# Kernel tuning notes

Measured on AMD Instinct MI355X. Metric: run time of the kernel, lower is better.

Reference implementation:

```python
import jax, jax.numpy as jnp
import numpy as np

B, S, D, H = 2, 2048, 1024, 16
DK = D // H

def setup_inputs() -> dict:
    key = jax.random.key(0)
    ks = jax.random.split(key, 12)
    scale = 1.0 / np.sqrt(D)
    inp = {
        'q': jax.random.normal(ks[0], (B, S, D), jnp.float32),
        'k': jax.random.normal(ks[1], (B, S, D), jnp.float32),
        'v': jax.random.normal(ks[2], (B, S, D), jnp.float32),
        # causal mask: 1 where attending is allowed (j <= i), 0 for future tokens
        'mask': jnp.tril(jnp.ones((S, S), jnp.int32))[None, None, :, :],
        'wq': jax.random.normal(ks[3], (D, D), jnp.float32) * scale,
        'bq': jnp.zeros((D,), jnp.float32),
        'wk': jax.random.normal(ks[4], (D, D), jnp.float32) * scale,
        'bk': jnp.zeros((D,), jnp.float32),
        'wv': jax.random.normal(ks[5], (D, D), jnp.float32) * scale,
        'bv': jnp.zeros((D,), jnp.float32),
        'wo': jax.random.normal(ks[6], (D, D), jnp.float32) * scale,
        'bo': jnp.zeros((D,), jnp.float32),
    }
    return inp


def reference(q, k, v, mask, wq, bq, wk, bk, wv, bv, wo, bo):
    def split_heads(x):
        # [B,S,D] -> [B,H,S,DK]
        return x.reshape(B, S, H, DK).transpose(0, 2, 1, 3)

    query = split_heads(q @ wq + bq)
    key_ = split_heads(k @ wk + bk)
    value = split_heads(v @ wv + bv)

    # [B,H,S,S] attention scores
    scores = jnp.einsum('bhqd,bhkd->bhqk', query, key_) / jnp.sqrt(
        jnp.asarray(DK, jnp.float32))
    scores = jnp.where(mask == 0, jnp.asarray(-1e9, scores.dtype), scores)
    attn = jax.nn.softmax(scores, axis=-1)  # dropout p=0.0 (eval mode)

    x = jnp.einsum('bhqk,bhkd->bhqd', attn, value)  # [B,H,S,DK]
    x = x.transpose(0, 2, 1, 3).reshape(B, S, D)
    return x @ wo + bo
```

## Files before the change

kernel.cpp:

```cpp
#include <hip/hip_runtime.h>
#include <hip/hip_bf16.h>

#define BATCH 2
#define SEQ   2048
#define DMODEL 1024
#define NHEAD 16
#define DK    64
#define MTOK  (BATCH * SEQ)

typedef __attribute__((ext_vector_type(8))) short bf16x8;
typedef __attribute__((ext_vector_type(4))) float f32x4;

__device__ __forceinline__ unsigned short f2bf(float x) {
    unsigned u = __float_as_uint(x);
    u = (u + 0x7FFFu + ((u >> 16) & 1u)) >> 16;
    return (unsigned short)u;
}

__device__ __forceinline__ void store_out(float* p, float v)          { *p = v; }
__device__ __forceinline__ void store_out(unsigned short* p, float v) { *p = f2bf(v); }

__device__ __forceinline__ void g2lds16(const void* g, void* l) {
    __builtin_amdgcn_global_load_lds(
        (const __attribute__((address_space(1))) void*)g,
        (__attribute__((address_space(3))) void*)l, 16, 0, 0);
}

__global__ __launch_bounds__(256) void cvt3_bf16_kernel(
    const float* __restrict__ s0, const float* __restrict__ s1,
    const float* __restrict__ s2,
    unsigned short* __restrict__ d0, unsigned short* __restrict__ d1,
    unsigned short* __restrict__ d2, int n)
{
    const float* src; unsigned short* dst;
    switch (blockIdx.z) {
        case 0:  src = s0; dst = d0; break;
        case 1:  src = s1; dst = d1; break;
        default: src = s2; dst = d2; break;
    }
    int i = (blockIdx.x * 256 + threadIdx.x) * 8;
    if (i >= n) return;
    float4 a = *(const float4*)(src + i);
    float4 b = *(const float4*)(src + i + 4);
    union { unsigned short s[8]; uint4 u; } o;
    o.s[0] = f2bf(a.x); o.s[1] = f2bf(a.y); o.s[2] = f2bf(a.z); o.s[3] = f2bf(a.w);
    o.s[4] = f2bf(b.x); o.s[5] = f2bf(b.y); o.s[6] = f2bf(b.z); o.s[7] = f2bf(b.w);
    *(uint4*)(dst + i) = o.u;
}

__global__ __launch_bounds__(256) void wtrans_kernel(
    const float* __restrict__ w0, const float* __restrict__ w1,
    const float* __restrict__ w2, const float* __restrict__ w3,
    unsigned short* __restrict__ t0, unsigned short* __restrict__ t1,
    unsigned short* __restrict__ t2, unsigned short* __restrict__ t3)
{
    __shared__ float tile[32][33];
    const float* W; unsigned short* T;
    switch (blockIdx.z) {
        case 0:  W = w0; T = t0; break;
        case 1:  W = w1; T = t1; break;
        case 2:  W = w2; T = t2; break;
        default: W = w3; T = t3; break;
    }
    const int n0 = blockIdx.x * 32, k0 = blockIdx.y * 32;
    const int t  = threadIdx.x;
    const int r  = t >> 3;
    const int c4 = (t & 7) * 4;

    float4 v = *(const float4*)&W[(size_t)(k0 + r) * DMODEL + n0 + c4];
    tile[r][c4 + 0] = v.x; tile[r][c4 + 1] = v.y;
    tile[r][c4 + 2] = v.z; tile[r][c4 + 3] = v.w;
    __syncthreads();

    union { unsigned short s[4]; uint2 u; } o;
#pragma unroll
    for (int u = 0; u < 4; ++u) o.s[u] = f2bf(tile[c4 + u][r]);
    *(uint2*)&T[(size_t)(n0 + r) * DMODEL + k0 + c4] = o.u;
}

struct Gemm3 {
    const unsigned short* A[3];
    const unsigned short* Bt[3];
    const float* bias[3];
    void* C[3];
};

template <typename OutT>
__global__ __launch_bounds__(256) void gemm_lds_kernel(Gemm3 g, int M, int N, int K)
{
    __shared__ unsigned short sA[16 * 512];
    __shared__ unsigned short sB[16 * 512];

    const int z = blockIdx.z;
    const unsigned short* __restrict__ A  = g.A[z];
    const unsigned short* __restrict__ Bt = g.Bt[z];
    const float* __restrict__ bias = g.bias[z];
    OutT* __restrict__ C = (OutT*)g.C[z];

    const int t    = threadIdx.x;
    const int w    = t >> 6;
    const int lane = t & 63;
    const int ln   = lane & 15;
    const int qg   = lane >> 4;
    const int wm   = w >> 1;
    const int wn   = w & 1;
    const int row0 = blockIdx.y * 128;
    const int col0 = blockIdx.x * 128;

    const unsigned short* sp[8];
    unsigned short* lp[8];
#pragma unroll
    for (int i = 0; i < 8; ++i) {
        const int s = w * 8 + i;
        if (s < 16) {
            const int mtg = s >> 1, kc = s & 1;
            sp[i] = A + (size_t)(row0 + mtg * 16 + ln) * K + kc * 32 + qg * 8;
            lp[i] = &sA[s * 512];
        } else {
            const int bi = s - 16;
            const int ntg = bi >> 1, kc = bi & 1;
            sp[i] = Bt + (size_t)(col0 + ntg * 16 + ln) * K + kc * 32 + qg * 8;
            lp[i] = &sB[bi * 512];
        }
    }

    f32x4 acc[4][4];
#pragma unroll
    for (int mt = 0; mt < 4; ++mt)
#pragma unroll
        for (int nt = 0; nt < 4; ++nt) acc[mt][nt] = (f32x4){0.f, 0.f, 0.f, 0.f};

    for (int kt = 0; kt < K / 64; ++kt) {
        __syncthreads();
        const int koff = kt * 64;
#pragma unroll
        for (int i = 0; i < 8; ++i)
            g2lds16(sp[i] + koff, lp[i]);
        __syncthreads();

#pragma unroll
        for (int kc = 0; kc < 2; ++kc) {
            bf16x8 aF[4], bF[4];
#pragma unroll
            for (int mt = 0; mt < 4; ++mt)
                aF[mt] = *(const bf16x8*)&sA[(((wm * 4 + mt) * 2) + kc) * 512 + lane * 8];
#pragma unroll
            for (int nt = 0; nt < 4; ++nt)
                bF[nt] = *(const bf16x8*)&sB[(((wn * 4 + nt) * 2) + kc) * 512 + lane * 8];
#pragma unroll
            for (int mt = 0; mt < 4; ++mt)
#pragma unroll
                for (int nt = 0; nt < 4; ++nt)
                    acc[mt][nt] = __builtin_amdgcn_mfma_f32_16x16x32_bf16(
                        aF[mt], bF[nt], acc[mt][nt], 0, 0, 0);
        }
    }

    float bfv[4];
#pragma unroll
    for (int nt = 0; nt < 4; ++nt)
        bfv[nt] = bias[col0 + wn * 64 + nt * 16 + ln];

#pragma unroll
    for (int mt = 0; mt < 4; ++mt)
#pragma unroll
        for (int nt = 0; nt < 4; ++nt)
#pragma unroll
            for (int r = 0; r < 4; ++r) {
                int row = row0 + wm * 64 + mt * 16 + qg * 4 + r;
                int col = col0 + wn * 64 + nt * 16 + ln;
                store_out(&C[(size_t)row * N + col], acc[mt][nt][r] + bfv[nt]);
            }
}

#define BR 64
#define BC 64
#define PSTR 72

__global__ __launch_bounds__(256, 4) void attn_mfma_kernel(
    const unsigned short* __restrict__ Qg, const unsigned short* __restrict__ Kg,
    const unsigned short* __restrict__ Vg, unsigned short* __restrict__ O)
{
    __shared__ unsigned short sQ[8 * 512];
    __shared__ unsigned short sK[8 * 512];
    __shared__ unsigned short sVt[DK * 64];
    __shared__ unsigned short sP[BR * PSTR];

    const int t    = threadIdx.x;
    const int w    = t >> 6;
    const int lane = t & 63;
    const int ln   = lane & 15;
    const int qg   = lane >> 4;

    const int id  = blockIdx.x;
    const int bh  = id & 31;
    const int qt  = (SEQ / BR - 1) - (id >> 5);
    const int b   = bh >> 4;
    const int h   = bh & 15;
    const int qi0 = qt * BR;

    const size_t rowbase = (size_t)b * SEQ;
    const size_t colbase = (size_t)h * DK;

#pragma unroll
    for (int i = 0; i < 2; ++i) {
        const int s = w * 2 + i;
        const unsigned short* gp =
            Qg + (rowbase + qi0 + w * 16 + ln) * DMODEL + colbase + i * 32 + qg * 8;
        g2lds16(gp, &sQ[s * 512]);
    }
    __syncthreads();

    bf16x8 aq[2];
#pragma unroll
    for (int kc = 0; kc < 2; ++kc)
        aq[kc] = *(const bf16x8*)&sQ[(w * 2 + kc) * 512 + lane * 8];

    f32x4 ofrag[4];
#pragma unroll
    for (int nt = 0; nt < 4; ++nt) ofrag[nt] = (f32x4){0.f, 0.f, 0.f, 0.f};
    float m_r[4], l_r[4];
#pragma unroll
    for (int r = 0; r < 4; ++r) { m_r[r] = -3.0e38f; l_r[r] = 0.f; }

    for (int j0 = 0; j0 <= qi0; j0 += BC) {
        __syncthreads();

#pragma unroll
        for (int i = 0; i < 2; ++i) {
            const int s  = w * 2 + i;
            const int nt = s >> 1, kc = s & 1;
            const unsigned short* gp =
                Kg + (rowbase + j0 + nt * 16 + ln) * DMODEL + colbase + kc * 32 + qg * 8;
            g2lds16(gp, &sK[s * 512]);
        }
#pragma unroll
        for (int it = 0; it < 2; ++it) {
            int chunk = t + 256 * it;
            int r  = chunk >> 3;
            int c  = (chunk & 7) * 8;
            int ci = chunk & 7;
            union { uint4 u; unsigned short s[8]; } d;
            d.u = *(const uint4*)&Vg[(rowbase + j0 + r) * DMODEL + colbase + c];
#pragma unroll
            for (int u = 0; u < 8; ++u)
                sVt[(c + u) * 64 + (r ^ (ci * 8))] = d.s[u];
        }
        __syncthreads();

        f32x4 sf[4];
#pragma unroll
        for (int nt = 0; nt < 4; ++nt) {
            f32x4 a2 = (f32x4){0.f, 0.f, 0.f, 0.f};
#pragma unroll
            for (int kc = 0; kc < 2; ++kc) {
                bf16x8 bk = *(const bf16x8*)&sK[(nt * 2 + kc) * 512 + lane * 8];
                a2 = __builtin_amdgcn_mfma_f32_16x16x32_bf16(aq[kc], bk, a2, 0, 0, 0);
            }
            sf[nt] = a2;
        }

        const bool diag = (j0 == qi0);
#pragma unroll
        for (int nt = 0; nt < 4; ++nt)
#pragma unroll
            for (int r = 0; r < 4; ++r) {
                float x = sf[nt][r] * 0.125f;
                if (diag) {
                    int qrow = w * 16 + qg * 4 + r;
                    int col  = nt * 16 + ln;
                    if (col > qrow) x = -3.0e38f;
                }
                sf[nt][r] = x;
            }

        float rmax[4];
#pragma unroll
        for (int r = 0; r < 4; ++r)
            rmax[r] = fmaxf(fmaxf(sf[0][r], sf[1][r]), fmaxf(sf[2][r], sf[3][r]));
#pragma unroll
        for (int off = 8; off >= 1; off >>= 1)
#pragma unroll
            for (int r = 0; r < 4; ++r)
                rmax[r] = fmaxf(rmax[r], __shfl_xor(rmax[r], off));

        float alpha[4];
#pragma unroll
        for (int r = 0; r < 4; ++r) {
            float mn = fmaxf(m_r[r], rmax[r]);
            alpha[r] = __expf(m_r[r] - mn);
            m_r[r] = mn;
        }

        float pf[4][4];
        float rsum[4] = {0.f, 0.f, 0.f, 0.f};
#pragma unroll
        for (int nt = 0; nt < 4; ++nt)
#pragma unroll
            for (int r = 0; r < 4; ++r) {
                float p = __expf(sf[nt][r] - m_r[r]);
                pf[nt][r] = p;
                rsum[r] += p;
            }
#pragma unroll
        for (int off = 8; off >= 1; off >>= 1)
#pragma unroll
            for (int r = 0; r < 4; ++r)
                rsum[r] += __shfl_xor(rsum[r], off);
#pragma unroll
        for (int r = 0; r < 4; ++r) l_r[r] = l_r[r] * alpha[r] + rsum[r];
#pragma unroll
        for (int nt = 0; nt < 4; ++nt)
#pragma unroll
            for (int r = 0; r < 4; ++r) ofrag[nt][r] *= alpha[r];

#pragma unroll
        for (int nt = 0; nt < 4; ++nt)
#pragma unroll
            for (int r = 0; r < 4; ++r) {
                int row = w * 16 + qg * 4 + r;
                int col = (nt * 16 + ln) ^ (((w * 4 + qg) & 7) * 8);
                sP[row * PSTR + col] = f2bf(pf[nt][r]);
            }

        bf16x8 apf[2];
#pragma unroll
        for (int kc = 0; kc < 2; ++kc) {
            int row = w * 16 + ln;
            int col = (kc * 32 + qg * 8) ^ ((((row >> 2) & 7)) * 8);
            apf[kc] = *(const bf16x8*)&sP[row * PSTR + col];
        }

#pragma unroll
        for (int nt = 0; nt < 4; ++nt) {
#pragma unroll
            for (int kc = 0; kc < 2; ++kc) {
                int dk = nt * 16 + ln;
                int ci = (dk >> 3) & 7;
                bf16x8 bv = *(const bf16x8*)&sVt[dk * 64 + ((kc * 32 + qg * 8) ^ (ci * 8))];
                ofrag[nt] = __builtin_amdgcn_mfma_f32_16x16x32_bf16(apf[kc], bv, ofrag[nt], 0, 0, 0);
            }
        }
    }

#pragma unroll
    for (int nt = 0; nt < 4; ++nt)
#pragma unroll
        for (int r = 0; r < 4; ++r) {
            int gq = qi0 + w * 16 + qg * 4 + r;
            O[(rowbase + gq) * DMODEL + colbase + nt * 16 + ln] =
                f2bf(ofrag[nt][r] / l_r[r]);
        }
}

extern "C" void kernel_launch(void* const* d_in, const int* in_sizes, int n_in,
                              void* d_out, int out_size, void* d_ws, size_t ws_size,
                              hipStream_t stream)
{
    const float* q  = (const float*)d_in[0];
    const float* k  = (const float*)d_in[1];
    const float* v  = (const float*)d_in[2];
    const float* wq = (const float*)d_in[4];
    const float* bq = (const float*)d_in[5];
    const float* wk = (const float*)d_in[6];
    const float* bk = (const float*)d_in[7];
    const float* wv = (const float*)d_in[8];
    const float* bv = (const float*)d_in[9];
    const float* wo = (const float*)d_in[10];
    const float* bo = (const float*)d_in[11];
    float* out = (float*)d_out;

    const size_t mat  = (size_t)MTOK * DMODEL;
    const size_t wmat = (size_t)DMODEL * DMODEL;
    unsigned short* Abq = (unsigned short*)d_ws;
    unsigned short* Abk = Abq + mat;
    unsigned short* Abv = Abk + mat;
    unsigned short* WtQ = Abv + mat;
    unsigned short* WtK = WtQ + wmat;
    unsigned short* WtV = WtK + wmat;
    unsigned short* WtO = WtV + wmat;
    unsigned short* Qb  = WtO + wmat;
    unsigned short* Kb  = Qb + mat;
    unsigned short* Vb  = Kb + mat;
    unsigned short* CTX = Vb + mat;

    cvt3_bf16_kernel<<<dim3((unsigned)(mat / 2048), 1, 3), 256, 0, stream>>>(
        q, k, v, Abq, Abk, Abv, (int)mat);
    wtrans_kernel<<<dim3(32, 32, 4), 256, 0, stream>>>(wq, wk, wv, wo, WtQ, WtK, WtV, WtO);

    Gemm3 gqkv;
    gqkv.A[0] = Abq; gqkv.A[1] = Abk; gqkv.A[2] = Abv;
    gqkv.Bt[0] = WtQ; gqkv.Bt[1] = WtK; gqkv.Bt[2] = WtV;
    gqkv.bias[0] = bq; gqkv.bias[1] = bk; gqkv.bias[2] = bv;
    gqkv.C[0] = Qb; gqkv.C[1] = Kb; gqkv.C[2] = Vb;
    gemm_lds_kernel<unsigned short><<<dim3(DMODEL / 128, MTOK / 128, 3), 256, 0, stream>>>(
        gqkv, MTOK, DMODEL, DMODEL);

    attn_mfma_kernel<<<BATCH * NHEAD * (SEQ / BR), 256, 0, stream>>>(Qb, Kb, Vb, CTX);

    Gemm3 go;
    go.A[0] = CTX; go.Bt[0] = WtO; go.bias[0] = bo; go.C[0] = out;
    go.A[1] = go.A[2] = nullptr; go.Bt[1] = go.Bt[2] = nullptr;
    go.bias[1] = go.bias[2] = nullptr; go.C[1] = go.C[2] = nullptr;
    gemm_lds_kernel<float><<<dim3(DMODEL / 128, MTOK / 128, 1), 256, 0, stream>>>(
        go, MTOK, DMODEL, DMODEL);
}
```

Measured before the change: 310.8 us.

## Double-buffer attention K/V, produce transposed V from GEMM, fold scale into Q

The V projection GEMM is computed as Wv^T·X^T so it writes V already transposed, which removes the scalar LDS transpose inside the attention loop. K and V tiles are now double-buffered with async global-to-LDS loads issued one tile ahead, leaving one barrier per iteration. The softmax scale and log2(e) are folded into the Q projection so the kernel can use exp2f, and the row sum comes from an MFMA against a ones vector instead of shuffles. The output GEMM uses a narrower 128x64 tile to launch more blocks. These changes raise LDS use and drop the occupancy hint on the attention kernel. Accumulating the row sum from bf16-rounded probabilities changes numerics slightly.

```diff
diff --git a/kernel.cpp b/kernel.cpp
--- a/kernel.cpp
+++ b/kernel.cpp
@@ -78,24 +78,33 @@
     *(uint2*)&T[(size_t)(n0 + r) * DMODEL + k0 + c4] = o.u;
 }
 
-struct Gemm3 {
-    const unsigned short* A[3];
-    const unsigned short* Bt[3];
-    const float* bias[3];
-    void* C[3];
+struct GemmP {
+    const unsigned short* A;
+    const unsigned short* Bt;
+    const float* bias;
+    void* C;
+    int N, K, ctShift, biasByRow;
+    float scale;
 };
-
-template <typename OutT>
-__global__ __launch_bounds__(256) void gemm_lds_kernel(Gemm3 g, int M, int N, int K)
+struct Gemm3 { GemmP p[3]; };
+
+template <typename OutT, int NTILE>
+__global__ __launch_bounds__(256) void gemm_lds_kernel(Gemm3 g)
 {
     __shared__ unsigned short sA[16 * 512];
-    __shared__ unsigned short sB[16 * 512];
-
-    const int z = blockIdx.z;
-    const unsigned short* __restrict__ A  = g.A[z];
-    const unsigned short* __restrict__ Bt = g.Bt[z];
-    const float* __restrict__ bias = g.bias[z];
-    OutT* __restrict__ C = (OutT*)g.C[z];
+    __shared__ unsigned short sB[4 * NTILE * 512];
+
+    const GemmP p = g.p[blockIdx.z];
+    const unsigned short* __restrict__ A  = p.A;
+    const unsigned short* __restrict__ Bt = p.Bt;
+    OutT* __restrict__ C = (OutT*)p.C;
+    const int K = p.K, N = p.N;
+
+    const int bid = blockIdx.x;
+    const int bx = bid & ((1 << p.ctShift) - 1);
+    const int by = bid >> p.ctShift;
+    const int row0 = by * 128;
+    const int col0 = bx * (NTILE * 32);
 
     const int t    = threadIdx.x;
     const int w    = t >> 6;
@@ -104,14 +113,13 @@
     const int qg   = lane >> 4;
     const int wm   = w >> 1;
     const int wn   = w & 1;
-    const int row0 = blockIdx.y * 128;
-    const int col0 = blockIdx.x * 128;
-
-    const unsigned short* sp[8];
-    unsigned short* lp[8];
-#pragma unroll
-    for (int i = 0; i < 8; ++i) {
-        const int s = w * 8 + i;
+
+    const int PW = 4 + NTILE;
+    const unsigned short* sp[PW];
+    unsigned short* lp[PW];
+#pragma unroll
+    for (int i = 0; i < PW; ++i) {
+        const int s = w * PW + i;
         if (s < 16) {
             const int mtg = s >> 1, kc = s & 1;
             sp[i] = A + (size_t)(row0 + mtg * 16 + ln) * K + kc * 32 + qg * 8;
@@ -124,52 +132,61 @@
         }
     }
 
-    f32x4 acc[4][4];
+    f32x4 acc[4][NTILE];
 #pragma unroll
     for (int mt = 0; mt < 4; ++mt)
 #pragma unroll
-        for (int nt = 0; nt < 4; ++nt) acc[mt][nt] = (f32x4){0.f, 0.f, 0.f, 0.f};
+        for (int nt = 0; nt < NTILE; ++nt) acc[mt][nt] = (f32x4){0.f, 0.f, 0.f, 0.f};
 
     for (int kt = 0; kt < K / 64; ++kt) {
         __syncthreads();
         const int koff = kt * 64;
 #pragma unroll
-        for (int i = 0; i < 8; ++i)
+        for (int i = 0; i < PW; ++i)
             g2lds16(sp[i] + koff, lp[i]);
         __syncthreads();
 
 #pragma unroll
         for (int kc = 0; kc < 2; ++kc) {
-            bf16x8 aF[4], bF[4];
+            bf16x8 aF[4], bF[NTILE];
 #pragma unroll
             for (int mt = 0; mt < 4; ++mt)
                 aF[mt] = *(const bf16x8*)&sA[(((wm * 4 + mt) * 2) + kc) * 512 + lane * 8];
 #pragma unroll
-            for (int nt = 0; nt < 4; ++nt)
-                bF[nt] = *(const bf16x8*)&sB[(((wn * 4 + nt) * 2) + kc) * 512 + lane * 8];
+            for (int nt = 0; nt < NTILE; ++nt)
+                bF[nt] = *(const bf16x8*)&sB[(((wn * NTILE + nt) * 2) + kc) * 512 + lane * 8];
 #pragma unroll
             for (int mt = 0; mt < 4; ++mt)
 #pragma unroll
-                for (int nt = 0; nt < 4; ++nt)
+                for (int nt = 0; nt < NTILE; ++nt)
                     acc[mt][nt] = __builtin_amdgcn_mfma_f32_16x16x32_bf16(
                         aF[mt], bF[nt], acc[mt][nt], 0, 0, 0);
         }
     }
 
-    float bfv[4];
-#pragma unroll
-    for (int nt = 0; nt < 4; ++nt)
-        bfv[nt] = bias[col0 + wn * 64 + nt * 16 + ln];
+    float bcol[NTILE], brow[4][4];
+    if (!p.biasByRow) {
+#pragma unroll
+        for (int nt = 0; nt < NTILE; ++nt)
+            bcol[nt] = p.bias[col0 + wn * NTILE * 16 + nt * 16 + ln];
+    } else {
+#pragma unroll
+        for (int mt = 0; mt < 4; ++mt)
+#pragma unroll
+            for (int r = 0; r < 4; ++r)
+                brow[mt][r] = p.bias[row0 + wm * 64 + mt * 16 + qg * 4 + r];
+    }
 
 #pragma unroll
     for (int mt = 0; mt < 4; ++mt)
 #pragma unroll
-        for (int nt = 0; nt < 4; ++nt)
+        for (int nt = 0; nt < NTILE; ++nt)
 #pragma unroll
             for (int r = 0; r < 4; ++r) {
                 int row = row0 + wm * 64 + mt * 16 + qg * 4 + r;
-                int col = col0 + wn * 64 + nt * 16 + ln;
-                store_out(&C[(size_t)row * N + col], acc[mt][nt][r] + bfv[nt]);
+                int col = col0 + wn * NTILE * 16 + nt * 16 + ln;
+                float bb = p.biasByRow ? brow[mt][r] : bcol[nt];
+                store_out(&C[(size_t)row * N + col], (acc[mt][nt][r] + bb) * p.scale);
             }
 }
 
@@ -177,13 +194,13 @@
 #define BC 64
 #define PSTR 72
 
-__global__ __launch_bounds__(256, 4) void attn_mfma_kernel(
+__global__ __launch_bounds__(256) void attn_mfma_kernel(
     const unsigned short* __restrict__ Qg, const unsigned short* __restrict__ Kg,
-    const unsigned short* __restrict__ Vg, unsigned short* __restrict__ O)
+    const unsigned short* __restrict__ VT, unsigned short* __restrict__ O)
 {
+    __shared__ unsigned short sK[2][8 * 512];
+    __shared__ unsigned short sV[2][8 * 512];
     __shared__ unsigned short sQ[8 * 512];
-    __shared__ unsigned short sK[8 * 512];
-    __shared__ unsigned short sVt[DK * 64];
     __shared__ unsigned short sP[BR * PSTR];
 
     const int t    = threadIdx.x;
@@ -205,9 +222,13 @@
 #pragma unroll
     for (int i = 0; i < 2; ++i) {
         const int s = w * 2 + i;
-        const unsigned short* gp =
-            Qg + (rowbase + qi0 + w * 16 + ln) * DMODEL + colbase + i * 32 + qg * 8;
-        g2lds16(gp, &sQ[s * 512]);
+        const int nt = s >> 1, kc = s & 1;
+        g2lds16(Qg + (rowbase + qi0 + w * 16 + ln) * DMODEL + colbase + i * 32 + qg * 8,
+                &sQ[s * 512]);
+        g2lds16(Kg + (rowbase + nt * 16 + ln) * DMODEL + colbase + kc * 32 + qg * 8,
+                &sK[0][s * 512]);
+        g2lds16(VT + (size_t)(colbase + nt * 16 + ln) * MTOK + rowbase + kc * 32 + qg * 8,
+                &sV[0][s * 512]);
     }
     __syncthreads();
 
@@ -216,37 +237,35 @@
     for (int kc = 0; kc < 2; ++kc)
         aq[kc] = *(const bf16x8*)&sQ[(w * 2 + kc) * 512 + lane * 8];
 
+    const short one_bf = (short)0x3F80;
+    const bf16x8 bone = (bf16x8){one_bf, one_bf, one_bf, one_bf,
+                                 one_bf, one_bf, one_bf, one_bf};
+
     f32x4 ofrag[4];
 #pragma unroll
     for (int nt = 0; nt < 4; ++nt) ofrag[nt] = (f32x4){0.f, 0.f, 0.f, 0.f};
-    float m_r[4], l_r[4];
-#pragma unroll
-    for (int r = 0; r < 4; ++r) { m_r[r] = -3.0e38f; l_r[r] = 0.f; }
-
-    for (int j0 = 0; j0 <= qi0; j0 += BC) {
-        __syncthreads();
-
-#pragma unroll
-        for (int i = 0; i < 2; ++i) {
-            const int s  = w * 2 + i;
-            const int nt = s >> 1, kc = s & 1;
-            const unsigned short* gp =
-                Kg + (rowbase + j0 + nt * 16 + ln) * DMODEL + colbase + kc * 32 + qg * 8;
-            g2lds16(gp, &sK[s * 512]);
-        }
-#pragma unroll
-        for (int it = 0; it < 2; ++it) {
-            int chunk = t + 256 * it;
-            int r  = chunk >> 3;
-            int c  = (chunk & 7) * 8;
-            int ci = chunk & 7;
-            union { uint4 u; unsigned short s[8]; } d;
-            d.u = *(const uint4*)&Vg[(rowbase + j0 + r) * DMODEL + colbase + c];
-#pragma unroll
-            for (int u = 0; u < 8; ++u)
-                sVt[(c + u) * 64 + (r ^ (ci * 8))] = d.s[u];
-        }
-        __syncthreads();
+    f32x4 osum = (f32x4){0.f, 0.f, 0.f, 0.f};
+    float m_r[4];
+#pragma unroll
+    for (int r = 0; r < 4; ++r) m_r[r] = -3.0e38f;
+
+    const int ntiles = qt + 1;
+    for (int jt = 0; jt < ntiles; ++jt) {
+        const int cur = jt & 1;
+
+        if (jt + 1 < ntiles) {
+            const int j1 = (jt + 1) * BC;
+            const int nb = cur ^ 1;
+#pragma unroll
+            for (int i = 0; i < 2; ++i) {
+                const int s = w * 2 + i;
+                const int nt = s >> 1, kc = s & 1;
+                g2lds16(Kg + (rowbase + j1 + nt * 16 + ln) * DMODEL + colbase + kc * 32 + qg * 8,
+                        &sK[nb][s * 512]);
+                g2lds16(VT + (size_t)(colbase + nt * 16 + ln) * MTOK + rowbase + j1 + kc * 32 + qg * 8,
+                        &sV[nb][s * 512]);
+            }
+        }
 
         f32x4 sf[4];
 #pragma unroll
@@ -254,25 +273,22 @@
             f32x4 a2 = (f32x4){0.f, 0.f, 0.f, 0.f};
 #pragma unroll
             for (int kc = 0; kc < 2; ++kc) {
-                bf16x8 bk = *(const bf16x8*)&sK[(nt * 2 + kc) * 512 + lane * 8];
+                bf16x8 bk = *(const bf16x8*)&sK[cur][(nt * 2 + kc) * 512 + lane * 8];
                 a2 = __builtin_amdgcn_mfma_f32_16x16x32_bf16(aq[kc], bk, a2, 0, 0, 0);
             }
             sf[nt] = a2;
         }
 
-        const bool diag = (j0 == qi0);
-#pragma unroll
-        for (int nt = 0; nt < 4; ++nt)
-#pragma unroll
-            for (int r = 0; r < 4; ++r) {
-                float x = sf[nt][r] * 0.125f;
-                if (diag) {
+        if (jt == ntiles - 1) {
+#pragma unroll
+            for (int nt = 0; nt < 4; ++nt)
+#pragma unroll
+                for (int r = 0; r < 4; ++r) {
                     int qrow = w * 16 + qg * 4 + r;
                     int col  = nt * 16 + ln;
-                    if (col > qrow) x = -3.0e38f;
+                    if (col > qrow) sf[nt][r] = -1.0e30f;
                 }
-                sf[nt][r] = x;
-            }
+        }
 
         float rmax[4];
 #pragma unroll
@@ -288,40 +304,26 @@
 #pragma unroll
         for (int r = 0; r < 4; ++r) {
             float mn = fmaxf(m_r[r], rmax[r]);
-            alpha[r] = __expf(m_r[r] - mn);
+            alpha[r] = exp2f(m_r[r] - mn);
             m_r[r] = mn;
         }
 
-        float pf[4][4];
-        float rsum[4] = {0.f, 0.f, 0.f, 0.f};
 #pragma unroll
         for (int nt = 0; nt < 4; ++nt)
 #pragma unroll
             for (int r = 0; r < 4; ++r) {
-                float p = __expf(sf[nt][r] - m_r[r]);
-                pf[nt][r] = p;
-                rsum[r] += p;
-            }
-#pragma unroll
-        for (int off = 8; off >= 1; off >>= 1)
-#pragma unroll
-            for (int r = 0; r < 4; ++r)
-                rsum[r] += __shfl_xor(rsum[r], off);
-#pragma unroll
-        for (int r = 0; r < 4; ++r) l_r[r] = l_r[r] * alpha[r] + rsum[r];
-#pragma unroll
-        for (int nt = 0; nt < 4; ++nt)
-#pragma unroll
-            for (int r = 0; r < 4; ++r) ofrag[nt][r] *= alpha[r];
-
-#pragma unroll
-        for (int nt = 0; nt < 4; ++nt)
-#pragma unroll
-            for (int r = 0; r < 4; ++r) {
+                float pv = exp2f(sf[nt][r] - m_r[r]);
                 int row = w * 16 + qg * 4 + r;
                 int col = (nt * 16 + ln) ^ (((w * 4 + qg) & 7) * 8);
-                sP[row * PSTR + col] = f2bf(pf[nt][r]);
+                sP[row * PSTR + col] = f2bf(pv);
             }
+
+#pragma unroll
+        for (int nt = 0; nt < 4; ++nt)
+#pragma unroll
+            for (int r = 0; r < 4; ++r) ofrag[nt][r] *= alpha[r];
+#pragma unroll
+        for (int r = 0; r < 4; ++r) osum[r] *= alpha[r];
 
         bf16x8 apf[2];
 #pragma unroll
@@ -332,24 +334,30 @@
         }
 
 #pragma unroll
+        for (int kc = 0; kc < 2; ++kc)
+            osum = __builtin_amdgcn_mfma_f32_16x16x32_bf16(apf[kc], bone, osum, 0, 0, 0);
+#pragma unroll
         for (int nt = 0; nt < 4; ++nt) {
 #pragma unroll
             for (int kc = 0; kc < 2; ++kc) {
-                int dk = nt * 16 + ln;
-                int ci = (dk >> 3) & 7;
-                bf16x8 bv = *(const bf16x8*)&sVt[dk * 64 + ((kc * 32 + qg * 8) ^ (ci * 8))];
+                bf16x8 bv = *(const bf16x8*)&sV[cur][(nt * 2 + kc) * 512 + lane * 8];
                 ofrag[nt] = __builtin_amdgcn_mfma_f32_16x16x32_bf16(apf[kc], bv, ofrag[nt], 0, 0, 0);
             }
         }
-    }
-
+
+        __syncthreads();
+    }
+
+    float inv[4];
+#pragma unroll
+    for (int r = 0; r < 4; ++r) inv[r] = 1.0f / osum[r];
 #pragma unroll
     for (int nt = 0; nt < 4; ++nt)
 #pragma unroll
         for (int r = 0; r < 4; ++r) {
             int gq = qi0 + w * 16 + qg * 4 + r;
             O[(rowbase + gq) * DMODEL + colbase + nt * 16 + ln] =
-                f2bf(ofrag[nt][r] / l_r[r]);
+                f2bf(ofrag[nt][r] * inv[r]);
         }
 }
 
@@ -381,27 +389,25 @@
     unsigned short* WtO = WtV + wmat;
     unsigned short* Qb  = WtO + wmat;
     unsigned short* Kb  = Qb + mat;
-    unsigned short* Vb  = Kb + mat;
-    unsigned short* CTX = Vb + mat;
+    unsigned short* VT  = Kb + mat;
+    unsigned short* CTX = VT + mat;
 
     cvt3_bf16_kernel<<<dim3((unsigned)(mat / 2048), 1, 3), 256, 0, stream>>>(
         q, k, v, Abq, Abk, Abv, (int)mat);
     wtrans_kernel<<<dim3(32, 32, 4), 256, 0, stream>>>(wq, wk, wv, wo, WtQ, WtK, WtV, WtO);
 
-    Gemm3 gqkv;
-    gqkv.A[0] = Abq; gqkv.A[1] = Abk; gqkv.A[2] = Abv;
-    gqkv.Bt[0] = WtQ; gqkv.Bt[1] = WtK; gqkv.Bt[2] = WtV;
-    gqkv.bias[0] = bq; gqkv.bias[1] = bk; gqkv.bias[2] = bv;
-    gqkv.C[0] = Qb; gqkv.C[1] = Kb; gqkv.C[2] = Vb;
-    gemm_lds_kernel<unsigned short><<<dim3(DMODEL / 128, MTOK / 128, 3), 256, 0, stream>>>(
-        gqkv, MTOK, DMODEL, DMODEL);
-
-    attn_mfma_kernel<<<BATCH * NHEAD * (SEQ / BR), 256, 0, stream>>>(Qb, Kb, Vb, CTX);
+    const float qscale = 0.125f * 1.44269504088896f;
+    Gemm3 g;
+    g.p[0] = (GemmP){Abq, WtQ, bq, (void*)Qb, DMODEL, DMODEL, 3, 0, qscale};
+    g.p[1] = (GemmP){Abk, WtK, bk, (void*)Kb, DMODEL, DMODEL, 3, 0, 1.0f};
+    g.p[2] = (GemmP){WtV, Abv, bv, (void*)VT, MTOK,   DMODEL, 5, 1, 1.0f};
+    gemm_lds_kernel<unsigned short, 4><<<dim3(256, 1, 3), 256, 0, stream>>>(g);
+
+    attn_mfma_kernel<<<BATCH * NHEAD * (SEQ / BR), 256, 0, stream>>>(Qb, Kb, VT, CTX);
 
     Gemm3 go;
-    go.A[0] = CTX; go.Bt[0] = WtO; go.bias[0] = bo; go.C[0] = out;
-    go.A[1] = go.A[2] = nullptr; go.Bt[1] = go.Bt[2] = nullptr;
-    go.bias[1] = go.bias[2] = nullptr; go.C[1] = go.C[2] = nullptr;
-    gemm_lds_kernel<float><<<dim3(DMODEL / 128, MTOK / 128, 1), 256, 0, stream>>>(
-        go, MTOK, DMODEL, DMODEL);
-}
+    go.p[0] = (GemmP){CTX, WtO, bo, (void*)out, DMODEL, DMODEL, 4, 0, 1.0f};
+    go.p[1] = go.p[0];
+    go.p[2] = go.p[0];
+    gemm_lds_kernel<float, 2><<<dim3(512, 1, 1), 256, 0, stream>>>(go);
+}
```

Result: faster. 272.6 us (-12.3%).
